# Optimization experiments

Hardware: AMD Instinct MI355X
Metric: run time of the kernel (lower is better)

## Reference

```python
import jax, jax.numpy as jnp
import numpy as np

N, F, E, C, CELL = 2048, 64, 4, 3, 15
OUT_CH, OUT_K, N_CLASS = 10, 15, 2


def _xex(X, A_attr, wx0, wx1, we):
    # pairwise score tensor: Y[i,j] = X[i]@wx0 + X[j]@wx1 + A_attr[i,j]@we -> [N,N,c_out]
    return (X @ wx0)[:, None, :] + (X @ wx1)[None, :, :] + jnp.einsum('ije,ec->ijc', A_attr, we)


def _gcn_layer(X, A, A_attr, ax0, ax1, ae, ix0, ix1, ie, gx0, gx1, ge, wr):
    n = X.shape[0]
    # multi-channel attention (MA) branch
    att = jax.nn.elu(_xex(X, A_attr, ax0, ax1, ae)) + 1.0001  # [n,n,C]
    att = att * A[:, :, None]
    att = jax.nn.softmax(att, axis=1)  # softmax over neighbor axis (incl. zeroed entries, as in TF code)
    att = att * A[:, :, None]
    y_node = jnp.einsum('ijc,jf->icf', att, X).reshape(n, -1)        # [n, C*F_in]
    y_edge = jnp.einsum('ijc,ije->ice', att, A_attr).reshape(n, -1)  # [n, C*E]
    # gated branch (unmasked sum over all j, as in aggr_neibors_gate)
    info = jnp.tanh(_xex(X, A_attr, ix0, ix1, ie))        # [n,n,CELL]
    gate = jax.nn.sigmoid(_xex(X, A_attr, gx0, gx1, ge))  # [n,n,CELL]
    y_gate = jnp.sum(info * gate, axis=1)                 # [n, CELL]
    r = jnp.concatenate([X, y_edge, y_node, y_gate], axis=1)
    return jnp.tanh(r @ wr + 0.1)


def _forward(X, A, A_attr,
             att0_x0, att0_x1, att0_e, info0_x0, info0_x1, info0_e,
             gate0_x0, gate0_x1, gate0_e, r0,
             att1_x0, att1_x1, att1_e, info1_x0, info1_x1, info1_e,
             gate1_x0, gate1_x1, gate1_e, r1,
             out_att, out_cnn, out_r):
    h0 = _gcn_layer(X, A, A_attr, att0_x0, att0_x1, att0_e,
                    info0_x0, info0_x1, info0_e, gate0_x0, gate0_x1, gate0_e, r0)
    h1 = _gcn_layer(h0, A, A_attr, att1_x0, att1_x1, att1_e,
                    info1_x0, info1_x1, info1_e, gate1_x0, gate1_x1, gate1_e, r1)
    Xc = jnp.concatenate([X, h0, h1], axis=1)       # [n, F + 2*CELL]
    att = jax.nn.softmax(Xc @ out_att, axis=0)      # node-wise attention pooling, [n, OUT_CH]
    image = att.T @ Xc                              # [OUT_CH, F + 2*CELL]
    image = jnp.tanh(image @ out_cnn + 0.1)         # [OUT_CH, OUT_K]
    logits = image.reshape(1, -1) @ out_r + 0.1
    return jax.nn.softmax(logits, axis=-1)          # [1, N_CLASS]


def setup_inputs() -> dict:
    keys = jax.random.split(jax.random.key(0), 26)
    tn = lambda k, s: jax.random.normal(k, s, jnp.float32) * 0.05  # truncated_normal init approx
    return {
        'X': jax.random.normal(keys[0], (N, F), jnp.float32),
        'A': (jax.random.uniform(keys[1], (N, N)) < 0.02).astype(jnp.float32),  # ~40 neighbors/node
        'A_attr': jax.random.normal(keys[2], (N, N, E), jnp.float32),
        'att0_x0': tn(keys[3], (F, C)), 'att0_x1': tn(keys[4], (F, C)), 'att0_e': tn(keys[5], (E, C)),
        'info0_x0': tn(keys[6], (F, CELL)), 'info0_x1': tn(keys[7], (F, CELL)), 'info0_e': tn(keys[8], (E, CELL)),
        'gate0_x0': tn(keys[9], (F, CELL)), 'gate0_x1': tn(keys[10], (F, CELL)), 'gate0_e': tn(keys[11], (E, CELL)),
        'r0': tn(keys[12], (F + (F + E) * C + CELL, CELL)),
        'att1_x0': tn(keys[13], (CELL, C)), 'att1_x1': tn(keys[14], (CELL, C)), 'att1_e': tn(keys[15], (E, C)),
        'info1_x0': tn(keys[16], (CELL, CELL)), 'info1_x1': tn(keys[17], (CELL, CELL)), 'info1_e': tn(keys[18], (E, CELL)),
        'gate1_x0': tn(keys[19], (CELL, CELL)), 'gate1_x1': tn(keys[20], (CELL, CELL)), 'gate1_e': tn(keys[21], (E, CELL)),
        'r1': tn(keys[22], (CELL + (CELL + E) * C + CELL, CELL)),
        'out_att': tn(keys[23], (F + 2 * CELL, OUT_CH)),
        'out_cnn': tn(keys[24], (F + 2 * CELL, OUT_K)),
        'out_r': tn(keys[25], (OUT_K * OUT_CH, N_CLASS)),
    }


def reference(X, A, A_attr,
              att0_x0, att0_x1, att0_e, info0_x0, info0_x1, info0_e,
              gate0_x0, gate0_x1, gate0_e, r0,
              att1_x0, att1_x1, att1_e, info1_x0, info1_x1, info1_e,
              gate1_x0, gate1_x1, gate1_e, r1,
              out_att, out_cnn, out_r):
    return _forward(X, A, A_attr,
                    att0_x0, att0_x1, att0_e, info0_x0, info0_x1, info0_e,
                    gate0_x0, gate0_x1, gate0_e, r0,
                    att1_x0, att1_x1, att1_e, info1_x0, info1_x1, info1_e,
                    gate1_x0, gate1_x1, gate1_e, r1,
                    out_att, out_cnn, out_r)
```

## Files before the change

### kernel.cpp

```cpp
#include <hip/hip_runtime.h>
#include <hip/hip_bf16.h>
#include <math.h>

#define NN 2048
#define EE 4
#define CC 3
#define CELL 15
#define MAXD 128
#define GATE_JZ 8

typedef unsigned short u16;
typedef float f32x2 __attribute__((ext_vector_type(2)));

__device__ __forceinline__ float b2f(u16 u) { return __uint_as_float(((unsigned int)u) << 16); }
__device__ __forceinline__ u16 f2b(float f) {
    unsigned int x = __float_as_uint(f);
    unsigned int r = (x + 0x7fffu + ((x >> 16) & 1u)) >> 16;
    return (u16)r;
}
__device__ __forceinline__ float fastrcp(float x) { return __builtin_amdgcn_rcpf(x); }
__device__ __forceinline__ float fastexp2(float x) { return __builtin_amdgcn_exp2f(x); }
__device__ __forceinline__ float rfl(float x) {
    return __uint_as_float(__builtin_amdgcn_readfirstlane(__float_as_uint(x)));
}
__device__ __forceinline__ float ldx(const void* p, size_t i, bool bf) {
    if (bf) return b2f(((const u16*)p)[i]);
    return ((const float*)p)[i];
}
__device__ __forceinline__ bool detect_bf(const u16* X) {
    int lane = threadIdx.x & 63;
    u16 u = X[2 * lane];
    int e = (u >> 7) & 0xFF;
    unsigned long long m = __ballot(e >= 100 && e <= 150);
    return __popcll(m) >= 32;
}

__global__ __launch_bounds__(256) void k_edges(const void* __restrict__ A, const u16* __restrict__ Xd,
                                               int* __restrict__ flag, int* __restrict__ deg,
                                               int* __restrict__ edges, float* __restrict__ imgp) {
    bool bf = detect_bf(Xd);
    if (blockIdx.x == 0) {
        if (threadIdx.x == 0) *flag = bf ? 1 : 0;
        for (int q = threadIdx.x; q < 940; q += 256) imgp[q] = 0.f;
    }
    int lane = threadIdx.x & 63, wv = threadIdx.x >> 6;
    int i = blockIdx.x * 4 + wv;
    int base = 0;
    for (int jb = 0; jb < NN; jb += 64) {
        float a = ldx(A, (size_t)i * NN + jb + lane, bf);
        unsigned long long m = __ballot(a != 0.f);
        if (a != 0.f) {
            int slot = base + __popcll(m & ((1ull << lane) - 1ull));
            if (slot < MAXD) edges[i * MAXD + slot] = jb + lane;
        }
        base += __popcll(m);
    }
    if (lane == 0) deg[i] = base;
}

template<int FIN, bool XRAW>
__global__ void k_proj(const int* __restrict__ flag, const void* __restrict__ Xin_,
                       const void* __restrict__ ax0, const void* __restrict__ ax1,
                       const void* __restrict__ ix0, const void* __restrict__ ix1,
                       const void* __restrict__ gx0, const void* __restrict__ gx1,
                       float* __restrict__ p0, float* __restrict__ pj,
                       float* __restrict__ pa0, float* __restrict__ pa1) {
    __shared__ float xs[FIN];
    bool bf = (*flag != 0);
    bool xbf = XRAW ? bf : false;
    int nd = blockIdx.x;
    int t = threadIdx.x;
    if (t < FIN) xs[t] = ldx(Xin_, (size_t)nd * FIN + t, xbf);
    __syncthreads();
    if (t >= 66) return;
    const void* W; int col, OUT; float* dst;
    if (t < 15)      { W = ix0; col = t;      OUT = CELL; dst = p0  + nd * 30 + t; }
    else if (t < 30) { W = gx0; col = t - 15; OUT = CELL; dst = p0  + nd * 30 + t; }
    else if (t < 45) { W = ix1; col = t - 30; OUT = CELL; dst = pj  + nd * 30 + (t - 30); }
    else if (t < 60) { W = gx1; col = t - 45; OUT = CELL; dst = pj  + nd * 30 + (t - 30); }
    else if (t < 63) { W = ax0; col = t - 60; OUT = CC;   dst = pa0 + nd * 3 + (t - 60); }
    else             { W = ax1; col = t - 63; OUT = CC;   dst = pa1 + nd * 3 + (t - 63); }
    float acc = 0.f;
    for (int f = 0; f < FIN; ++f) acc += xs[f] * ldx(W, (size_t)f * OUT + col, bf);
    *dst = acc;
}

template<int FIN, bool BF, bool XRAW>
__device__ void att_body(const void* __restrict__ Xin_, const void* __restrict__ A_attr,
                         const void* __restrict__ ae,
                         const float* __restrict__ pa0, const float* __restrict__ pa1,
                         const int* __restrict__ deg, const int* __restrict__ edges,
                         float* __restrict__ y_node, float* __restrict__ y_edge,
                         float (*ew)[4], float* pdn, float* pne, float* pnn) {
    int i = blockIdx.x;
    int t = threadIdx.x;
    int lane = t & 63, wv = t >> 6;
    float aew[EE][CC];
    #pragma unroll
    for (int e = 0; e < EE; ++e)
        #pragma unroll
        for (int c = 0; c < CC; ++c) aew[e][c] = ldx(ae, e * CC + c, BF);
    float pa0v[3] = { pa0[i*3], pa0[i*3+1], pa0[i*3+2] };
    int dg = deg[i]; if (dg > MAXD) dg = MAXD;
    float dn[3] = {0.f, 0.f, 0.f};
    float ne[3][4] = {{0.f}};
    for (int base = 0; base < dg; base += 256) {
        int idx = base + t;
        if (idx < dg) {
            int j = edges[i * MAXD + idx];
            float a0, a1, a2, a3;
            if (BF) {
                const u16* ap = (const u16*)A_attr + ((size_t)i * NN + j) * EE;
                ushort4 av = *(const ushort4*)ap;
                a0 = b2f(av.x); a1 = b2f(av.y); a2 = b2f(av.z); a3 = b2f(av.w);
            } else {
                const float* ap = (const float*)A_attr + ((size_t)i * NN + j) * EE;
                float4 av = *(const float4*)ap;
                a0 = av.x; a1 = av.y; a2 = av.z; a3 = av.w;
            }
            float w[3];
            #pragma unroll
            for (int c = 0; c < 3; ++c) {
                float s = pa0v[c] + pa1[j*3 + c]
                        + a0*aew[0][c] + a1*aew[1][c] + a2*aew[2][c] + a3*aew[3][c];
                float val = (s > 0.f) ? (s + 1.0001f) : (__expf(s) - 1.f + 1.0001f);
                float wc = __expf(val);
                w[c] = wc;
                dn[c] += wc;
                ne[c][0] += wc * a0; ne[c][1] += wc * a1; ne[c][2] += wc * a2; ne[c][3] += wc * a3;
            }
            ew[idx][0] = __int_as_float(j);
            ew[idx][1] = w[0]; ew[idx][2] = w[1]; ew[idx][3] = w[2];
        }
    }
    #pragma unroll
    for (int off = 32; off; off >>= 1) {
        #pragma unroll
        for (int c = 0; c < 3; ++c) {
            dn[c] += __shfl_xor(dn[c], off);
            #pragma unroll
            for (int e = 0; e < 4; ++e) ne[c][e] += __shfl_xor(ne[c][e], off);
        }
    }
    if (lane == 0) {
        #pragma unroll
        for (int c = 0; c < 3; ++c) {
            pdn[wv*3 + c] = dn[c];
            #pragma unroll
            for (int e = 0; e < 4; ++e) pne[(wv*3 + c)*4 + e] = ne[c][e];
        }
    }
    __syncthreads();
    float rdn[3];
    #pragma unroll
    for (int c = 0; c < 3; ++c) {
        float s = (float)(NN - dg);
        #pragma unroll
        for (int w2 = 0; w2 < 4; ++w2) s += pdn[w2*3 + c];
        rdn[c] = 1.f / s;
    }
    float nn0 = 0.f, nn1 = 0.f, nn2 = 0.f;
    bool xbf = XRAW ? BF : false;
    if constexpr (FIN == 15) {
        int sub = lane >> 4, f = lane & 15;
        for (int idx = wv * 4 + sub; idx < dg; idx += 16) {
            int j = __float_as_int(ew[idx][0]);
            float w0 = ew[idx][1], w1 = ew[idx][2], w2 = ew[idx][3];
            if (f < 15) {
                float x = ldx(Xin_, (size_t)j * 15 + f, xbf);
                nn0 += w0 * x; nn1 += w1 * x; nn2 += w2 * x;
            }
        }
        pnn[(wv*3 + 0)*64 + lane] = nn0;
        pnn[(wv*3 + 1)*64 + lane] = nn1;
        pnn[(wv*3 + 2)*64 + lane] = nn2;
    } else {
        for (int idx = wv; idx < dg; idx += 4) {
            int j = __float_as_int(ew[idx][0]);
            float w0 = ew[idx][1], w1 = ew[idx][2], w2 = ew[idx][3];
            if (lane < FIN) {
                float x = ldx(Xin_, (size_t)j * FIN + lane, xbf);
                nn0 += w0 * x; nn1 += w1 * x; nn2 += w2 * x;
            }
        }
        if (lane < FIN) {
            pnn[(wv*3 + 0)*64 + lane] = nn0;
            pnn[(wv*3 + 1)*64 + lane] = nn1;
            pnn[(wv*3 + 2)*64 + lane] = nn2;
        }
    }
    __syncthreads();
    if constexpr (FIN == 15) {
        if (t < 15) {
            #pragma unroll
            for (int c = 0; c < 3; ++c) {
                float s = 0.f;
                #pragma unroll
                for (int w2 = 0; w2 < 4; ++w2)
                    #pragma unroll
                    for (int sb = 0; sb < 4; ++sb)
                        s += pnn[(w2*3 + c)*64 + sb*16 + t];
                y_node[(size_t)i * 45 + c*15 + t] = s * rdn[c];
            }
        }
    } else {
        if (t < FIN) {
            #pragma unroll
            for (int c = 0; c < 3; ++c) {
                float s = pnn[(0*3+c)*64 + t] + pnn[(1*3+c)*64 + t]
                        + pnn[(2*3+c)*64 + t] + pnn[(3*3+c)*64 + t];
                y_node[(size_t)i * (3*FIN) + c*FIN + t] = s * rdn[c];
            }
        }
    }
    if (t == 0) {
        #pragma unroll
        for (int c = 0; c < 3; ++c)
            #pragma unroll
            for (int e = 0; e < 4; ++e) {
                float s = pne[(0*3+c)*4+e] + pne[(1*3+c)*4+e] + pne[(2*3+c)*4+e] + pne[(3*3+c)*4+e];
                y_edge[(size_t)i * 12 + c*4 + e] = s * rdn[c];
            }
    }
}

template<int FIN, bool XRAW>
__global__ __launch_bounds__(256) void k_att(
        const int* __restrict__ flag,
        const void* __restrict__ Xin_, const void* __restrict__ A_attr, const void* __restrict__ ae,
        const float* __restrict__ pa0, const float* __restrict__ pa1,
        const int* __restrict__ deg, const int* __restrict__ edges,
        float* __restrict__ y_node, float* __restrict__ y_edge) {
    __shared__ float ew[MAXD][4];
    __shared__ float pdn[4*3];
    __shared__ float pne[4*3*4];
    __shared__ float pnn[4*3*64];
    if (*flag) att_body<FIN, true,  XRAW>(Xin_, A_attr, ae, pa0, pa1, deg, edges, y_node, y_edge, ew, pdn, pne, pnn);
    else       att_body<FIN, false, XRAW>(Xin_, A_attr, ae, pa0, pa1, deg, edges, y_node, y_edge, ew, pdn, pne, pnn);
}

template<bool BF, int K0, int NK>
__device__ void gate_half(const void* __restrict__ A_attr,
                          const void* __restrict__ iew, const void* __restrict__ gew,
                          const float* __restrict__ p0, const float* __restrict__ pj,
                          float* __restrict__ ygp, float* lds) {
    constexpr int T = 128;
    constexpr int JCH = NN / GATE_JZ;
    constexpr float L2E = 1.4426950408889634f;
    const int lane = threadIdx.x & 63;
    const int i = blockIdx.x * 4 + (threadIdx.x >> 6);
    const int jb0 = blockIdx.z * JCH;

    f32x2 W2[EE][NK];
    #pragma unroll
    for (int e = 0; e < EE; ++e)
        #pragma unroll
        for (int k = 0; k < NK; ++k) {
            W2[e][k].x = rfl(ldx(iew, e*CELL + K0 + k, BF) * (-2.f * L2E));
            W2[e][k].y = rfl(ldx(gew, e*CELL + K0 + k, BF) * (-L2E));
        }
    f32x2 p0p[NK];
    #pragma unroll
    for (int k = 0; k < NK; ++k) {
        p0p[k].x = rfl(p0[(size_t)i*30 + K0 + k] * (-2.f * L2E));
        p0p[k].y = rfl(p0[(size_t)i*30 + 15 + K0 + k] * (-L2E));
    }
    float acc[NK] = {0.f};

    for (int tb = jb0; tb < jb0 + JCH; tb += T) {
        __syncthreads();
        #pragma unroll
        for (int s = 0; s < 8; ++s) {
            int q = threadIdx.x + 256 * s;
            int r = q >> 4, c = q & 15;
            if (c < 2 * NK) {
                int k = c >> 1, comp = c & 1;
                float scale = comp ? (-L2E) : (-2.f * L2E);
                int ksrc = comp ? (15 + K0 + k) : (K0 + k);
                lds[r * 18 + c] = pj[(size_t)(tb + r) * 30 + ksrc] * scale;
            }
        }
        __syncthreads();
        #pragma unroll
        for (int js = 0; js < T; js += 64) {
            int r = js + lane;
            int j = tb + r;
            float a0, a1, a2, a3;
            if (BF) {
                const u16* ap = (const u16*)A_attr + ((size_t)i * NN + j) * EE;
                ushort4 av = *(const ushort4*)ap;
                a0 = b2f(av.x); a1 = b2f(av.y); a2 = b2f(av.z); a3 = b2f(av.w);
            } else {
                const float* ap = (const float*)A_attr + ((size_t)i * NN + j) * EE;
                float4 av = *(const float4*)ap;
                a0 = av.x; a1 = av.y; a2 = av.z; a3 = av.w;
            }
            f32x2 aa0 = {a0, a0}, aa1 = {a1, a1}, aa2 = {a2, a2}, aa3 = {a3, a3};
            const float* rowp = lds + r * 18;
            #pragma unroll
            for (int k = 0; k < NK; ++k) {
                f32x2 tu = *(const f32x2*)(rowp + 2*k) + p0p[k];
                tu += aa0 * W2[0][k];
                tu += aa1 * W2[1][k];
                tu += aa2 * W2[2][k];
                tu += aa3 * W2[3][k];
                float e1 = fastexp2(tu.x);
                float e2 = fastexp2(tu.y);
                float d1 = 1.f + e1, d2 = 1.f + e2;
                acc[k] = fmaf(1.f - e1, fastrcp(d1 * d2), acc[k]);
            }
        }
    }
    #pragma unroll
    for (int off = 32; off; off >>= 1)
        #pragma unroll
        for (int k = 0; k < NK; ++k) acc[k] += __shfl_xor(acc[k], off);
    if (lane == 0) {
        #pragma unroll
        for (int k = 0; k < NK; ++k)
            ygp[((size_t)blockIdx.z * NN + i) * CELL + K0 + k] = acc[k];
    }
}

__global__ __launch_bounds__(256, 2) void k_gate(
        const int* __restrict__ flag,
        const void* __restrict__ A_attr, const void* __restrict__ iew, const void* __restrict__ gew,
        const float* __restrict__ p0, const float* __restrict__ pj, float* __restrict__ ygp) {
    __shared__ __align__(16) float lds[128 * 18];
    if (*flag) {
        if (blockIdx.y == 0) gate_half<true, 0, 8>(A_attr, iew, gew, p0, pj, ygp, lds);
        else                 gate_half<true, 8, 7>(A_attr, iew, gew, p0, pj, ygp, lds);
    } else {
        if (blockIdx.y == 0) gate_half<false, 0, 8>(A_attr, iew, gew, p0, pj, ygp, lds);
        else                 gate_half<false, 8, 7>(A_attr, iew, gew, p0, pj, ygp, lds);
    }
}

__global__ __launch_bounds__(256) void k_hp(const int* __restrict__ flag,
        const void* __restrict__ X, const float* __restrict__ y_edge,
        const float* __restrict__ y_node, const float* __restrict__ y_gate,
        const void* __restrict__ wr,
        const void* __restrict__ ax0, const void* __restrict__ ax1,
        const void* __restrict__ ix0, const void* __restrict__ ix1,
        const void* __restrict__ gx0, const void* __restrict__ gx1,
        float* __restrict__ h0,
        float* __restrict__ p0o, float* __restrict__ pjo,
        float* __restrict__ pa0o, float* __restrict__ pa1o) {
    __shared__ float v[283];
    __shared__ float part[CELL][16];
    __shared__ float hs[CELL];
    bool bf = (*flag != 0);
    int nd = blockIdx.x, t = threadIdx.x;
    for (int q = t; q < 64; q += 256)  v[q]       = ldx(X, (size_t)nd * 64 + q, bf);
    for (int q = t; q < 12; q += 256)  v[64 + q]  = y_edge[(size_t)nd * 12 + q];
    for (int q = t; q < 192; q += 256) v[76 + q]  = y_node[(size_t)nd * 192 + q];
    for (int q = t; q < 15; q += 256) {
        float s = 0.f;
        #pragma unroll
        for (int z = 0; z < GATE_JZ; ++z) s += y_gate[((size_t)z * NN + nd) * CELL + q];
        v[268 + q] = s;
    }
    __syncthreads();
    if (t < 240) {
        int k = t >> 4, sub = t & 15;
        float acc = 0.f;
        for (int r = sub; r < 283; r += 16) acc += v[r] * ldx(wr, (size_t)r * CELL + k, bf);
        part[k][sub] = acc;
    }
    __syncthreads();
    if (t < CELL) {
        float acc = 0.1f;
        #pragma unroll
        for (int s = 0; s < 16; ++s) acc += part[t][s];
        float hv = tanhf(acc);
        hs[t] = hv;
        h0[(size_t)nd * CELL + t] = hv;
    }
    __syncthreads();
    if (t < 66) {
        const void* W; int col, OUT; float* dst;
        if (t < 15)      { W = ix0; col = t;      OUT = CELL; dst = p0o  + nd * 30 + t; }
        else if (t < 30) { W = gx0; col = t - 15; OUT = CELL; dst = p0o  + nd * 30 + t; }
        else if (t < 45) { W = ix1; col = t - 30; OUT = CELL; dst = pjo  + nd * 30 + (t - 30); }
        else if (t < 60) { W = gx1; col = t - 45; OUT = CELL; dst = pjo  + nd * 30 + (t - 30); }
        else if (t < 63) { W = ax0; col = t - 60; OUT = CC;   dst = pa0o + nd * 3 + (t - 60); }
        else             { W = ax1; col = t - 63; OUT = CC;   dst = pa1o + nd * 3 + (t - 63); }
        float acc = 0.f;
        for (int f = 0; f < CELL; ++f) acc += hs[f] * ldx(W, (size_t)f * OUT + col, bf);
        *dst = acc;
    }
}

__global__ __launch_bounds__(256) void k_hf(const int* __restrict__ flag,
        const void* __restrict__ X, const float* __restrict__ h0,
        const float* __restrict__ y_edge, const float* __restrict__ y_node,
        const float* __restrict__ y_gate, const void* __restrict__ wr,
        const void* __restrict__ oatt,
        float* __restrict__ h1, float* __restrict__ P) {
    __shared__ float v[87];
    __shared__ float xv[64];
    __shared__ float part[CELL][16];
    __shared__ float hs[CELL];
    __shared__ float pp[10][16];
    bool bf = (*flag != 0);
    int nd = blockIdx.x, t = threadIdx.x;
    for (int q = t; q < 15; q += 256) v[q]      = h0[(size_t)nd * 15 + q];
    for (int q = t; q < 12; q += 256) v[15 + q] = y_edge[(size_t)nd * 12 + q];
    for (int q = t; q < 45; q += 256) v[27 + q] = y_node[(size_t)nd * 45 + q];
    for (int q = t; q < 15; q += 256) {
        float s = 0.f;
        #pragma unroll
        for (int z = 0; z < GATE_JZ; ++z) s += y_gate[((size_t)z * NN + nd) * CELL + q];
        v[72 + q] = s;
    }
    for (int q = t; q < 64; q += 256) xv[q]     = ldx(X, (size_t)nd * 64 + q, bf);
    __syncthreads();
    if (t < 240) {
        int k = t >> 4, sub = t & 15;
        float acc = 0.f;
        for (int r = sub; r < 87; r += 16) acc += v[r] * ldx(wr, (size_t)r * CELL + k, bf);
        part[k][sub] = acc;
    }
    __syncthreads();
    if (t < CELL) {
        float acc = 0.1f;
        #pragma unroll
        for (int s = 0; s < 16; ++s) acc += part[t][s];
        float hv = tanhf(acc);
        hs[t] = hv;
        h1[(size_t)nd * CELL + t] = hv;
    }
    __syncthreads();
    if (t < 160) {
        int c = t >> 4, sub = t & 15;
        float acc = 0.f;
        for (int d = sub; d < 94; d += 16) {
            float x = (d < 64) ? xv[d] : (d < 79) ? v[d - 64] : hs[d - 79];
            acc += x * ldx(oatt, (size_t)d * 10 + c, bf);
        }
        pp[c][sub] = acc;
    }
    __syncthreads();
    if (t < 10) {
        float acc = 0.f;
        #pragma unroll
        for (int s = 0; s < 16; ++s) acc += pp[t][s];
        P[(size_t)nd * 10 + t] = acc;
    }
}

__global__ __launch_bounds__(1024) void k_f3(const int* __restrict__ flag,
                     const void* __restrict__ X, const float* __restrict__ h0,
                     const float* __restrict__ h1, const float* __restrict__ P,
                     float* __restrict__ image_pre) {
    __shared__ float red[16][10];
    __shared__ float wsl[32][10];
    bool bf = (*flag != 0);
    int t = threadIdx.x; int lane = t & 63; int wv = t >> 6;
    float mx[10], sm[10];
    #pragma unroll
    for (int c = 0; c < 10; ++c) mx[c] = -1e30f;
    for (int n = t; n < NN; n += 1024)
        #pragma unroll
        for (int c = 0; c < 10; ++c) mx[c] = fmaxf(mx[c], P[(size_t)n*10 + c]);
    #pragma unroll
    for (int off = 32; off; off >>= 1)
        #pragma unroll
        for (int c = 0; c < 10; ++c) mx[c] = fmaxf(mx[c], __shfl_xor(mx[c], off));
    if (lane == 0)
        #pragma unroll
        for (int c = 0; c < 10; ++c) red[wv][c] = mx[c];
    __syncthreads();
    #pragma unroll
    for (int c = 0; c < 10; ++c) {
        float m = red[0][c];
        for (int w2 = 1; w2 < 16; ++w2) m = fmaxf(m, red[w2][c]);
        mx[c] = m;
    }
    __syncthreads();
    #pragma unroll
    for (int c = 0; c < 10; ++c) sm[c] = 0.f;
    for (int n = t; n < NN; n += 1024)
        #pragma unroll
        for (int c = 0; c < 10; ++c) sm[c] += __expf(P[(size_t)n*10 + c] - mx[c]);
    #pragma unroll
    for (int off = 32; off; off >>= 1)
        #pragma unroll
        for (int c = 0; c < 10; ++c) sm[c] += __shfl_xor(sm[c], off);
    if (lane == 0)
        #pragma unroll
        for (int c = 0; c < 10; ++c) red[wv][c] = sm[c];
    __syncthreads();
    float rs[10];
    #pragma unroll
    for (int c = 0; c < 10; ++c) {
        float s = 0.f;
        for (int w2 = 0; w2 < 16; ++w2) s += red[w2][c];
        rs[c] = 1.f / s;
    }
    int n0 = blockIdx.x * 32;
    if (t < 320) {
        int nl = t / 10, c = t - nl * 10;
        wsl[nl][c] = __expf(P[(size_t)(n0 + nl)*10 + c] - mx[c]) * rs[c];
    }
    __syncthreads();
    if (t < 940) {
        int ch = t / 94, d = t - ch * 94;
        float acc = 0.f;
        for (int nl = 0; nl < 32; ++nl) {
            int n = n0 + nl;
            float w = wsl[nl][ch];
            float x = (d < 64) ? ldx(X, (size_t)n*64 + d, bf)
                    : (d < 79) ? h0[(size_t)n*15 + (d - 64)]
                               : h1[(size_t)n*15 + (d - 79)];
            acc += w * x;
        }
        atomicAdd(&image_pre[t], acc);
    }
}

__global__ __launch_bounds__(256) void k_f4(const int* __restrict__ flag,
                     const float* __restrict__ image_pre,
                     const void* __restrict__ out_cnn, const void* __restrict__ out_r,
                     void* __restrict__ out) {
    bool bf = (*flag != 0);
    __shared__ float ip[940];
    __shared__ float img2[150];
    __shared__ float red[8];
    int t = threadIdx.x;
    for (int q = t; q < 940; q += 256) ip[q] = image_pre[q];
    __syncthreads();
    if (t < 150) {
        int ch = t / 15, kk = t - ch * 15;
        float acc = 0.1f;
        for (int d = 0; d < 94; ++d) acc += ip[ch*94 + d] * ldx(out_cnn, (size_t)d*15 + kk, bf);
        img2[t] = tanhf(acc);
    }
    __syncthreads();
    float c0 = 0.f, c1 = 0.f;
    if (t < 150) {
        float vv = img2[t];
        c0 = vv * ldx(out_r, (size_t)t*2, bf);
        c1 = vv * ldx(out_r, (size_t)t*2 + 1, bf);
    }
    #pragma unroll
    for (int off = 32; off; off >>= 1) { c0 += __shfl_xor(c0, off); c1 += __shfl_xor(c1, off); }
    if ((t & 63) == 0) { red[(t >> 6)*2] = c0; red[(t >> 6)*2 + 1] = c1; }
    __syncthreads();
    if (t == 0) {
        float l0 = 0.1f + red[0] + red[2] + red[4] + red[6];
        float l1 = 0.1f + red[1] + red[3] + red[5] + red[7];
        float m = fmaxf(l0, l1);
        float e0 = __expf(l0 - m), e1 = __expf(l1 - m);
        float s = e0 + e1;
        float p0v = e0 / s, p1v = e1 / s;
        if (bf) { u16* o = (u16*)out; o[0] = f2b(p0v); o[1] = f2b(p1v); }
        else    { float* o = (float*)out; o[0] = p0v; o[1] = p1v; }
    }
}

extern "C" void kernel_launch(void* const* d_in, const int* in_sizes, int n_in,
                              void* d_out, int out_size, void* d_ws, size_t ws_size,
                              hipStream_t stream) {
    (void)in_sizes; (void)n_in; (void)out_size; (void)ws_size;
    const void* X      = d_in[0];
    const void* A      = d_in[1];
    const void* Aattr  = d_in[2];
    const void* a0x0 = d_in[3],  *a0x1 = d_in[4],  *a0e = d_in[5];
    const void* i0x0 = d_in[6],  *i0x1 = d_in[7],  *i0e = d_in[8];
    const void* g0x0 = d_in[9],  *g0x1 = d_in[10], *g0e = d_in[11];
    const void* r0   = d_in[12];
    const void* a1x0 = d_in[13], *a1x1 = d_in[14], *a1e = d_in[15];
    const void* i1x0 = d_in[16], *i1x1 = d_in[17], *i1e = d_in[18];
    const void* g1x0 = d_in[19], *g1x1 = d_in[20], *g1e = d_in[21];
    const void* r1   = d_in[22];
    const void* oatt = d_in[23], *ocnn = d_in[24], *orr = d_in[25];

    char* p = (char*)d_ws;
    auto alloc = [&](size_t bytes) -> void* { void* r = (void*)p; p += (bytes + 255) & ~(size_t)255; return r; };
    int*   flag   = (int*)  alloc(4);
    int*   deg    = (int*)  alloc(NN * 4);
    int*   edges  = (int*)  alloc((size_t)NN * MAXD * 4);
    float* p0_0   = (float*)alloc((size_t)NN * 30 * 4);
    float* pj_0   = (float*)alloc((size_t)NN * 30 * 4);
    float* pa0_0  = (float*)alloc((size_t)NN * 3 * 4);
    float* pa1_0  = (float*)alloc((size_t)NN * 3 * 4);
    float* p0_1   = (float*)alloc((size_t)NN * 30 * 4);
    float* pj_1   = (float*)alloc((size_t)NN * 30 * 4);
    float* pa0_1  = (float*)alloc((size_t)NN * 3 * 4);
    float* pa1_1  = (float*)alloc((size_t)NN * 3 * 4);
    float* ye0    = (float*)alloc((size_t)NN * 12 * 4);
    float* yn0    = (float*)alloc((size_t)NN * 192 * 4);
    float* yg0    = (float*)alloc((size_t)GATE_JZ * NN * CELL * 4);
    float* h0     = (float*)alloc((size_t)NN * CELL * 4);
    float* ye1    = (float*)alloc((size_t)NN * 12 * 4);
    float* yn1    = (float*)alloc((size_t)NN * 45 * 4);
    float* yg1    = (float*)alloc((size_t)GATE_JZ * NN * CELL * 4);
    float* h1     = (float*)alloc((size_t)NN * CELL * 4);
    float* P      = (float*)alloc((size_t)NN * 10 * 4);
    float* imgp   = (float*)alloc(940 * 4);

    k_edges<<<NN / 4, 256, 0, stream>>>(A, (const u16*)X, flag, deg, edges, imgp);

    dim3 ggate(NN / 4, 2, GATE_JZ);

    k_proj<64, true><<<NN, 128, 0, stream>>>(flag, X, a0x0, a0x1, i0x0, i0x1, g0x0, g0x1, p0_0, pj_0, pa0_0, pa1_0);
    k_att<64, true><<<NN, 256, 0, stream>>>(flag, X, Aattr, a0e, pa0_0, pa1_0, deg, edges, yn0, ye0);
    k_gate<<<ggate, 256, 0, stream>>>(flag, Aattr, i0e, g0e, p0_0, pj_0, yg0);
    k_hp<<<NN, 256, 0, stream>>>(flag, X, ye0, yn0, yg0, r0,
                                 a1x0, a1x1, i1x0, i1x1, g1x0, g1x1,
                                 h0, p0_1, pj_1, pa0_1, pa1_1);

    k_att<15, false><<<NN, 256, 0, stream>>>(flag, h0, Aattr, a1e, pa0_1, pa1_1, deg, edges, yn1, ye1);
    k_gate<<<ggate, 256, 0, stream>>>(flag, Aattr, i1e, g1e, p0_1, pj_1, yg1);
    k_hf<<<NN, 256, 0, stream>>>(flag, X, h0, ye1, yn1, yg1, r1, oatt, h1, P);

    k_f3<<<64, 1024, 0, stream>>>(flag, X, h0, h1, P, imgp);
    k_f4<<<1, 256, 0, stream>>>(flag, imgp, ocnn, orr, d_out);
}
```

Baseline: 358.7 us.

## Stage whole j-chunk of gate projections in LDS once per block of eight rows

The gate kernel now uses 512-thread blocks covering 8 rows i, with the j range split into 4 chunks instead of 8. Each block loads its full 512-row slice of scaled pj projections into shared memory once, with a single barrier, rather than re-staging 128-row tiles with two barriers per tile. This cuts redundant pj loads and synchronisation and halves the partial-sum count. In exchange it uses more LDS per block (about 36 KB) and launches fewer blocks, which may lower occupancy.

```diff
diff --git a/kernel.cpp b/kernel.cpp
--- a/kernel.cpp
+++ b/kernel.cpp
@@ -7,7 +7,7 @@
 #define CC 3
 #define CELL 15
 #define MAXD 128
-#define GATE_JZ 8
+#define GATE_JZ 4
 
 typedef unsigned short u16;
 typedef float f32x2 __attribute__((ext_vector_type(2)));
@@ -240,17 +240,27 @@
 }
 
 template<bool BF, int K0, int NK>
-__device__ void gate_half(const void* __restrict__ A_attr,
+__device__ void gate_body(const void* __restrict__ A_attr,
                           const void* __restrict__ iew, const void* __restrict__ gew,
                           const float* __restrict__ p0, const float* __restrict__ pj,
                           float* __restrict__ ygp, float* lds) {
-    constexpr int T = 128;
     constexpr int JCH = NN / GATE_JZ;
     constexpr float L2E = 1.4426950408889634f;
     const int lane = threadIdx.x & 63;
-    const int i = blockIdx.x * 4 + (threadIdx.x >> 6);
+    const int wv = threadIdx.x >> 6;
+    const int i = blockIdx.x * 8 + wv;
     const int jb0 = blockIdx.z * JCH;
 
+    {
+        int r = threadIdx.x;
+        const float* src = pj + (size_t)(jb0 + r) * 30;
+        float* dst = lds + r * 18;
+        #pragma unroll
+        for (int k = 0; k < NK; ++k) {
+            dst[2*k]     = src[K0 + k]      * (-2.f * L2E);
+            dst[2*k + 1] = src[15 + K0 + k] * (-L2E);
+        }
+    }
     f32x2 W2[EE][NK];
     #pragma unroll
     for (int e = 0; e < EE; ++e)
@@ -265,50 +275,36 @@
         p0p[k].x = rfl(p0[(size_t)i*30 + K0 + k] * (-2.f * L2E));
         p0p[k].y = rfl(p0[(size_t)i*30 + 15 + K0 + k] * (-L2E));
     }
+    __syncthreads();
+
     float acc[NK] = {0.f};
-
-    for (int tb = jb0; tb < jb0 + JCH; tb += T) {
-        __syncthreads();
-        #pragma unroll
-        for (int s = 0; s < 8; ++s) {
-            int q = threadIdx.x + 256 * s;
-            int r = q >> 4, c = q & 15;
-            if (c < 2 * NK) {
-                int k = c >> 1, comp = c & 1;
-                float scale = comp ? (-L2E) : (-2.f * L2E);
-                int ksrc = comp ? (15 + K0 + k) : (K0 + k);
-                lds[r * 18 + c] = pj[(size_t)(tb + r) * 30 + ksrc] * scale;
-            }
-        }
-        __syncthreads();
-        #pragma unroll
-        for (int js = 0; js < T; js += 64) {
-            int r = js + lane;
-            int j = tb + r;
-            float a0, a1, a2, a3;
-            if (BF) {
-                const u16* ap = (const u16*)A_attr + ((size_t)i * NN + j) * EE;
-                ushort4 av = *(const ushort4*)ap;
-                a0 = b2f(av.x); a1 = b2f(av.y); a2 = b2f(av.z); a3 = b2f(av.w);
-            } else {
-                const float* ap = (const float*)A_attr + ((size_t)i * NN + j) * EE;
-                float4 av = *(const float4*)ap;
-                a0 = av.x; a1 = av.y; a2 = av.z; a3 = av.w;
-            }
-            f32x2 aa0 = {a0, a0}, aa1 = {a1, a1}, aa2 = {a2, a2}, aa3 = {a3, a3};
-            const float* rowp = lds + r * 18;
-            #pragma unroll
-            for (int k = 0; k < NK; ++k) {
-                f32x2 tu = *(const f32x2*)(rowp + 2*k) + p0p[k];
-                tu += aa0 * W2[0][k];
-                tu += aa1 * W2[1][k];
-                tu += aa2 * W2[2][k];
-                tu += aa3 * W2[3][k];
-                float e1 = fastexp2(tu.x);
-                float e2 = fastexp2(tu.y);
-                float d1 = 1.f + e1, d2 = 1.f + e2;
-                acc[k] = fmaf(1.f - e1, fastrcp(d1 * d2), acc[k]);
-            }
+    #pragma unroll 2
+    for (int jg = 0; jg < JCH; jg += 64) {
+        int r = jg + lane;
+        int j = jb0 + r;
+        float a0, a1, a2, a3;
+        if (BF) {
+            const u16* ap = (const u16*)A_attr + ((size_t)i * NN + j) * EE;
+            ushort4 av = *(const ushort4*)ap;
+            a0 = b2f(av.x); a1 = b2f(av.y); a2 = b2f(av.z); a3 = b2f(av.w);
+        } else {
+            const float* ap = (const float*)A_attr + ((size_t)i * NN + j) * EE;
+            float4 av = *(const float4*)ap;
+            a0 = av.x; a1 = av.y; a2 = av.z; a3 = av.w;
+        }
+        f32x2 aa0 = {a0, a0}, aa1 = {a1, a1}, aa2 = {a2, a2}, aa3 = {a3, a3};
+        const float* rowp = lds + r * 18;
+        #pragma unroll
+        for (int k = 0; k < NK; ++k) {
+            f32x2 tu = *(const f32x2*)(rowp + 2*k) + p0p[k];
+            tu += aa0 * W2[0][k];
+            tu += aa1 * W2[1][k];
+            tu += aa2 * W2[2][k];
+            tu += aa3 * W2[3][k];
+            float e1 = fastexp2(tu.x);
+            float e2 = fastexp2(tu.y);
+            float d1 = 1.f + e1, d2 = 1.f + e2;
+            acc[k] = fmaf(1.f - e1, fastrcp(d1 * d2), acc[k]);
         }
     }
     #pragma unroll
@@ -322,17 +318,17 @@
     }
 }
 
-__global__ __launch_bounds__(256, 2) void k_gate(
+__global__ __launch_bounds__(512, 2) void k_gate(
         const int* __restrict__ flag,
         const void* __restrict__ A_attr, const void* __restrict__ iew, const void* __restrict__ gew,
         const float* __restrict__ p0, const float* __restrict__ pj, float* __restrict__ ygp) {
-    __shared__ __align__(16) float lds[128 * 18];
+    __shared__ __align__(16) float lds[512 * 18];
     if (*flag) {
-        if (blockIdx.y == 0) gate_half<true, 0, 8>(A_attr, iew, gew, p0, pj, ygp, lds);
-        else                 gate_half<true, 8, 7>(A_attr, iew, gew, p0, pj, ygp, lds);
+        if (blockIdx.y == 0) gate_body<true, 0, 8>(A_attr, iew, gew, p0, pj, ygp, lds);
+        else                 gate_body<true, 8, 7>(A_attr, iew, gew, p0, pj, ygp, lds);
     } else {
-        if (blockIdx.y == 0) gate_half<false, 0, 8>(A_attr, iew, gew, p0, pj, ygp, lds);
-        else                 gate_half<false, 8, 7>(A_attr, iew, gew, p0, pj, ygp, lds);
+        if (blockIdx.y == 0) gate_body<false, 0, 8>(A_attr, iew, gew, p0, pj, ygp, lds);
+        else                 gate_body<false, 8, 7>(A_attr, iew, gew, p0, pj, ygp, lds);
     }
 }
 
@@ -602,17 +598,17 @@
 
     k_edges<<<NN / 4, 256, 0, stream>>>(A, (const u16*)X, flag, deg, edges, imgp);
 
-    dim3 ggate(NN / 4, 2, GATE_JZ);
+    dim3 ggate(NN / 8, 2, GATE_JZ);
 
     k_proj<64, true><<<NN, 128, 0, stream>>>(flag, X, a0x0, a0x1, i0x0, i0x1, g0x0, g0x1, p0_0, pj_0, pa0_0, pa1_0);
     k_att<64, true><<<NN, 256, 0, stream>>>(flag, X, Aattr, a0e, pa0_0, pa1_0, deg, edges, yn0, ye0);
-    k_gate<<<ggate, 256, 0, stream>>>(flag, Aattr, i0e, g0e, p0_0, pj_0, yg0);
+    k_gate<<<ggate, 512, 0, stream>>>(flag, Aattr, i0e, g0e, p0_0, pj_0, yg0);
     k_hp<<<NN, 256, 0, stream>>>(flag, X, ye0, yn0, yg0, r0,
                                  a1x0, a1x1, i1x0, i1x1, g1x0, g1x1,
                                  h0, p0_1, pj_1, pa0_1, pa1_1);
 
     k_att<15, false><<<NN, 256, 0, stream>>>(flag, h0, Aattr, a1e, pa0_1, pa1_1, deg, edges, yn1, ye1);
-    k_gate<<<ggate, 256, 0, stream>>>(flag, Aattr, i1e, g1e, p0_1, pj_1, yg1);
+    k_gate<<<ggate, 512, 0, stream>>>(flag, Aattr, i1e, g1e, p0_1, pj_1, yg1);
     k_hf<<<NN, 256, 0, stream>>>(flag, X, h0, ye1, yn1, yg1, r1, oatt, h1, P);
 
     k_f3<<<64, 1024, 0, stream>>>(flag, X, h0, h1, P, imgp);
```

After: 360.4 us. Within noise of the previous version (+0.5%).
